# Performance work log

Hardware: AMD Instinct MI355X
Metric: run time of the kernel (lower is better)

Reference implementation:

```python
import jax, jax.numpy as jnp
import numpy as np
import math

B, L, S = 2, 2048, 2048
DIN, DK, DV, DOUT, H = 512, 512, 512, 512, 8
HEAD_SIZE = DK / H  # attention_head_size = dim_key_query_all / num_attention_heads


def setup_inputs() -> dict:
    key = jax.random.key(0)
    ks = jax.random.split(key, 12)
    inv = 1.0 / math.sqrt(DIN)
    return {
        "queries": jax.random.normal(ks[0], (B, L, DIN), jnp.float32),
        "keys": jax.random.normal(ks[1], (B, S, DIN), jnp.float32),
        "values": jax.random.normal(ks[2], (B, S, DIN), jnp.float32),
        "attn_mask": 0,
        "Wq": jax.random.uniform(ks[3], (DK, DIN), jnp.float32, -inv, inv),
        "Wk": jax.random.uniform(ks[4], (DK, DIN), jnp.float32, -inv, inv),
        "Wv": jax.random.uniform(ks[5], (DV, DIN), jnp.float32, -inv, inv),
        "bv": jax.random.uniform(ks[6], (DV,), jnp.float32, -inv, inv),
        "Wcb": jax.random.uniform(ks[7], (H, DIN), jnp.float32, -inv, inv),
        "mixing": 0.2 * jax.random.normal(ks[8], (H, DK), jnp.float32),
        "Wd": jax.random.uniform(ks[9], (DOUT, DV), jnp.float32, -1.0 / math.sqrt(DV), 1.0 / math.sqrt(DV)),
        "bd": jax.random.uniform(ks[10], (DOUT,), jnp.float32, -1.0 / math.sqrt(DV), 1.0 / math.sqrt(DV)),
    }


def reference(queries, keys, values, attn_mask, Wq, Wk, Wv, bv, Wcb, mixing, Wd, bd):
    # projections
    q = jnp.einsum('bld,ed->ble', queries, Wq)            # [B,L,DK]
    k = jnp.einsum('bsd,ed->bse', keys, Wk)               # [B,S,DK]
    v = jnp.einsum('bsd,ed->bse', values, Wv) + bv        # [B,S,DV]
    v = v.reshape(B, S, H, DV // H).transpose(0, 2, 1, 3)  # [B,H,S,dv]
    # collaborative scores: (q * mixing_h) @ k^T, per head
    mixed_q = q[:, None, :, :] * mixing[None, :, None, :]  # [B,H,L,DK]
    scores = jnp.einsum('bhle,bse->bhls', mixed_q, k)      # [B,H,L,S]
    # content bias: keys -> [B,S,H] -> broadcast over queries
    cb = jnp.einsum('bsd,hd->bhs', keys, Wcb)              # [B,H,S]
    scores = (scores + cb[:, :, None, :]) / math.sqrt(HEAD_SIZE)
    probs = jax.nn.softmax(scores, axis=-1)                # dropout p=0 (eval)
    ctx = jnp.einsum('bhls,bhsv->bhlv', probs, v)          # [B,H,L,dv]
    ctx = ctx.transpose(0, 2, 1, 3).reshape(B, L, DV)      # [B,L,DV]
    out = jnp.einsum('blv,ov->blo', ctx, Wd) + bd          # [B,L,DOUT]
    return out, probs
```

## Files before the change

kernel.cpp:

```cpp
#include <hip/hip_runtime.h>

typedef unsigned short u16;
typedef __bf16 bf16x8 __attribute__((ext_vector_type(8)));
typedef float floatx4 __attribute__((ext_vector_type(4)));

#define B_ 2
#define L_ 2048
#define S_ 2048
#define D_ 512
#define H_ 8

static __device__ __forceinline__ u16 f2bf(float f) {
  union { float f; unsigned u; } v; v.f = f;
  unsigned u = v.u;
  return (u16)((u + 0x7FFFu + ((u >> 16) & 1u)) >> 16);
}
static __device__ __forceinline__ float bf2f(u16 h) {
  union { unsigned u; float f; } v; v.u = ((unsigned)h) << 16;
  return v.f;
}

static __device__ __forceinline__ void gload16(const void* g, void* l) {
  __builtin_amdgcn_global_load_lds(
      (const __attribute__((address_space(1))) void*)g,
      (__attribute__((address_space(3))) void*)l, 16, 0, 0);
}

__global__ __launch_bounds__(256) void qkv_gemm(
    const float* __restrict__ Qin, const float* __restrict__ Kin, const float* __restrict__ Vin,
    const float* __restrict__ Wq, const float* __restrict__ Wk, const float* __restrict__ Wv,
    const float* __restrict__ bv,
    u16* __restrict__ qo, u16* __restrict__ ko, u16* __restrict__ vo)
{
  __shared__ u16 As[128][72];
  __shared__ u16 Bs[128][72];
  const int z = blockIdx.z;
  const float* A = (z == 0) ? Qin : (z == 1) ? Kin : Vin;
  const float* W = (z == 0) ? Wq : (z == 1) ? Wk : Wv;
  const int tid = threadIdx.x;
  const int m0 = blockIdx.y * 128;
  const int n0 = blockIdx.x * 128;
  const int lane = tid & 63, w = tid >> 6;
  const int ml = lane & 15, kl = lane >> 4;
  const int mqw = (w >> 1) * 64, nq = (w & 1) * 64;
  const int srow = tid >> 4, scg = tid & 15;

  floatx4 acc[4][4] = {};

  for (int k0 = 0; k0 < 512; k0 += 64) {
#pragma unroll
    for (int i = 0; i < 8; ++i) {
      const int r = srow + i * 16;
      float4 av = *(const float4*)&A[(size_t)(m0 + r) * 512 + k0 + scg * 4];
      ushort4 ua; ua.x = f2bf(av.x); ua.y = f2bf(av.y); ua.z = f2bf(av.z); ua.w = f2bf(av.w);
      *(ushort4*)&As[r][scg * 4] = ua;
      float4 wv = *(const float4*)&W[(size_t)(n0 + r) * 512 + k0 + scg * 4];
      ushort4 uw; uw.x = f2bf(wv.x); uw.y = f2bf(wv.y); uw.z = f2bf(wv.z); uw.w = f2bf(wv.w);
      *(ushort4*)&Bs[r][scg * 4] = uw;
    }
    __syncthreads();
#pragma unroll
    for (int kk = 0; kk < 64; kk += 32) {
      bf16x8 af[4], bfv[4];
#pragma unroll
      for (int i = 0; i < 4; ++i) af[i] = *(const bf16x8*)&As[mqw + i * 16 + ml][kk + kl * 8];
#pragma unroll
      for (int j = 0; j < 4; ++j) bfv[j] = *(const bf16x8*)&Bs[nq + j * 16 + ml][kk + kl * 8];
#pragma unroll
      for (int i = 0; i < 4; ++i)
#pragma unroll
        for (int j = 0; j < 4; ++j)
          acc[i][j] = __builtin_amdgcn_mfma_f32_16x16x32_bf16(af[i], bfv[j], acc[i][j], 0, 0, 0);
    }
    __syncthreads();
  }
#pragma unroll
  for (int i = 0; i < 4; ++i)
#pragma unroll
    for (int j = 0; j < 4; ++j) {
      const int gc = n0 + nq + j * 16 + ml;
#pragma unroll
      for (int r = 0; r < 4; ++r) {
        const int gr = m0 + mqw + i * 16 + kl * 4 + r;
        float v = acc[i][j][r];
        if (z == 0)      qo[(size_t)gr * 512 + gc] = f2bf(v);
        else if (z == 1) ko[(size_t)gr * 512 + gc] = f2bf(v);
        else             vo[(size_t)gr * 512 + gc] = f2bf(v + bv[gc]);
      }
    }
}

__global__ __launch_bounds__(256) void mixq_kernel(
    const u16* __restrict__ qb, const float* __restrict__ mixing, u16* __restrict__ mq)
{
  __shared__ float mixs[8 * 512];
  const int tid = threadIdx.x;
#pragma unroll
  for (int i = 0; i < 4; ++i)
    *(float4*)&mixs[(tid + i * 256) * 4] = *(const float4*)&mixing[(tid + i * 256) * 4];
  __syncthreads();
  const size_t unit = (size_t)blockIdx.x * 256 + tid;
  const size_t el = unit * 8;
  const int e = (int)(el & 511);
  const size_t bl = el >> 9;
  const int b = (int)(bl >> 11);
  const int l = (int)(bl & 2047);
  uint4 qv = *(const uint4*)&qb[el];
  const float q0 = bf2f((u16)(qv.x & 0xFFFFu)), q1 = bf2f((u16)(qv.x >> 16));
  const float q2 = bf2f((u16)(qv.y & 0xFFFFu)), q3 = bf2f((u16)(qv.y >> 16));
  const float q4 = bf2f((u16)(qv.z & 0xFFFFu)), q5 = bf2f((u16)(qv.z >> 16));
  const float q6 = bf2f((u16)(qv.w & 0xFFFFu)), q7 = bf2f((u16)(qv.w >> 16));
#pragma unroll
  for (int h = 0; h < 8; ++h) {
    const float* mp = &mixs[h * 512 + e];
    uint4 o;
    o.x = (unsigned)f2bf(q0 * mp[0]) | ((unsigned)f2bf(q1 * mp[1]) << 16);
    o.y = (unsigned)f2bf(q2 * mp[2]) | ((unsigned)f2bf(q3 * mp[3]) << 16);
    o.z = (unsigned)f2bf(q4 * mp[4]) | ((unsigned)f2bf(q5 * mp[5]) << 16);
    o.w = (unsigned)f2bf(q6 * mp[6]) | ((unsigned)f2bf(q7 * mp[7]) << 16);
    *(uint4*)&mq[(((size_t)b * 8 + h) * 2048 + l) * 512 + e] = o;
  }
}

__global__ __launch_bounds__(256) void out_gemm(
    const float* __restrict__ A0, const float* __restrict__ A1,
    const float* __restrict__ W,
    const float* __restrict__ bias, float* __restrict__ out)
{
  __shared__ u16 As[128][72];
  __shared__ u16 Bs[128][72];
  const int tid = threadIdx.x;
  const int m0 = blockIdx.y * 128;
  const int n0 = blockIdx.x * 128;
  const int lane = tid & 63, w = tid >> 6;
  const int ml = lane & 15, kl = lane >> 4;
  const int mqw = (w >> 1) * 64, nq = (w & 1) * 64;
  const int srow = tid >> 4, scg = tid & 15;

  floatx4 acc[4][4] = {};

  for (int k0 = 0; k0 < 512; k0 += 64) {
#pragma unroll
    for (int i = 0; i < 8; ++i) {
      const int r = srow + i * 16;
      const size_t aoff = (size_t)(m0 + r) * 512 + k0 + scg * 4;
      float4 a0 = *(const float4*)&A0[aoff];
      float4 a1 = *(const float4*)&A1[aoff];
      ushort4 ua;
      ua.x = f2bf(a0.x + a1.x); ua.y = f2bf(a0.y + a1.y);
      ua.z = f2bf(a0.z + a1.z); ua.w = f2bf(a0.w + a1.w);
      *(ushort4*)&As[r][scg * 4] = ua;
      float4 wv = *(const float4*)&W[(size_t)(n0 + r) * 512 + k0 + scg * 4];
      ushort4 uw; uw.x = f2bf(wv.x); uw.y = f2bf(wv.y); uw.z = f2bf(wv.z); uw.w = f2bf(wv.w);
      *(ushort4*)&Bs[r][scg * 4] = uw;
    }
    __syncthreads();
#pragma unroll
    for (int kk = 0; kk < 64; kk += 32) {
      bf16x8 af[4], bfv[4];
#pragma unroll
      for (int i = 0; i < 4; ++i) af[i] = *(const bf16x8*)&As[mqw + i * 16 + ml][kk + kl * 8];
#pragma unroll
      for (int j = 0; j < 4; ++j) bfv[j] = *(const bf16x8*)&Bs[nq + j * 16 + ml][kk + kl * 8];
#pragma unroll
      for (int i = 0; i < 4; ++i)
#pragma unroll
        for (int j = 0; j < 4; ++j)
          acc[i][j] = __builtin_amdgcn_mfma_f32_16x16x32_bf16(af[i], bfv[j], acc[i][j], 0, 0, 0);
    }
    __syncthreads();
  }
#pragma unroll
  for (int i = 0; i < 4; ++i)
#pragma unroll
    for (int j = 0; j < 4; ++j) {
      const int gc = n0 + nq + j * 16 + ml;
#pragma unroll
      for (int r = 0; r < 4; ++r) {
        const int gr = m0 + mqw + i * 16 + kl * 4 + r;
        out[(size_t)gr * 512 + gc] = acc[i][j][r] + bias[gc];
      }
    }
}

__global__ __launch_bounds__(256) void prep_kernel(
    const float* __restrict__ keys, const float* __restrict__ Wcb, float* __restrict__ cbuf,
    const u16* __restrict__ vb, u16* __restrict__ vT)
{
  __shared__ float Wl[8 * 512];
  __shared__ u16 t[64][72];
  const int tid = threadIdx.x;
  if (blockIdx.x < 1024) {
#pragma unroll
    for (int i = 0; i < 4; ++i) {
      const int idx = tid + i * 256;
      *(float4*)&Wl[idx * 4] = *(const float4*)&Wcb[idx * 4];
    }
    __syncthreads();
    const int w = tid >> 6, lane = tid & 63;
    const int rowid = blockIdx.x * 4 + w;
    const int b = rowid >> 11, s = rowid & 2047;
    const float* kr = keys + (size_t)rowid * 512;
    float acc[8] = {0.f, 0.f, 0.f, 0.f, 0.f, 0.f, 0.f, 0.f};
    for (int e = lane; e < 512; e += 64) {
      const float kv = kr[e];
#pragma unroll
      for (int hh = 0; hh < 8; ++hh) acc[hh] += kv * Wl[hh * 512 + e];
    }
#pragma unroll
    for (int hh = 0; hh < 8; ++hh) {
#pragma unroll
      for (int off = 32; off > 0; off >>= 1) acc[hh] += __shfl_xor(acc[hh], off, 64);
    }
    if (lane == 0) {
#pragma unroll
      for (int hh = 0; hh < 8; ++hh)
        cbuf[((size_t)b * 8 + hh) * 2048 + s] = acc[hh];
    }
  } else {
    const int id = blockIdx.x - 1024;
    const int b = id >> 8;
    const int rem = id & 255;
    const int s0 = (rem >> 3) * 64;
    const int e0 = (rem & 7) * 64;
    const int rr = tid >> 3, g = tid & 7;
#pragma unroll
    for (int i = 0; i < 2; ++i) {
      const int r = rr + i * 32;
      *(uint4*)&t[r][g * 8] = *(const uint4*)&vb[((size_t)b * S_ + s0 + r) * 512 + e0 + g * 8];
    }
    __syncthreads();
#pragma unroll
    for (int i = 0; i < 2; ++i) {
      const int er = rr + i * 32;
      uint4 o;
      o.x = (unsigned)t[g * 8 + 0][er] | ((unsigned)t[g * 8 + 1][er] << 16);
      o.y = (unsigned)t[g * 8 + 2][er] | ((unsigned)t[g * 8 + 3][er] << 16);
      o.z = (unsigned)t[g * 8 + 4][er] | ((unsigned)t[g * 8 + 5][er] << 16);
      o.w = (unsigned)t[g * 8 + 6][er] | ((unsigned)t[g * 8 + 7][er] << 16);
      *(uint4*)&vT[((size_t)b * 512 + e0 + er) * S_ + s0 + g * 8] = o;
    }
  }
}

template<int BF16OUT>
__global__ __launch_bounds__(256) void scores_gemm(
    const u16* __restrict__ mq, const u16* __restrict__ kb,
    const float* __restrict__ cbuf, float* __restrict__ sc, u16* __restrict__ sb)
{
  __shared__ u16 As[128][64];
  __shared__ u16 Bs[128][64];
  const int tid = threadIdx.x;
  const int bh = blockIdx.z, b = bh >> 3;
  const int m0 = blockIdx.y * 128;
  const int n0 = blockIdx.x * 128;
  const u16* mqb = mq + (size_t)bh * L_ * 512;
  const u16* kbb = kb + (size_t)b * S_ * 512;
  const int lane = tid & 63, w = tid >> 6;
  const int ml = lane & 15, kl = lane >> 4;
  const int mqw = (w >> 1) * 64, nq = (w & 1) * 64;
  const int lr = lane >> 3;
  const int lc = (lane & 7) * 8;

  floatx4 acc[4][4] = {};

  for (int k0 = 0; k0 < 512; k0 += 64) {
#pragma unroll
    for (int i = 0; i < 4; ++i) {
      const int c = w * 4 + i;
      const int r = c * 8 + lr;
      gload16(&mqb[(size_t)(m0 + r) * 512 + k0 + lc], &As[c * 8][0]);
      gload16(&kbb[(size_t)(n0 + r) * 512 + k0 + lc], &Bs[c * 8][0]);
    }
    __syncthreads();
#pragma unroll
    for (int kk = 0; kk < 64; kk += 32) {
      bf16x8 af[4], bfv[4];
#pragma unroll
      for (int i = 0; i < 4; ++i) af[i] = *(const bf16x8*)&As[mqw + i * 16 + ml][kk + kl * 8];
#pragma unroll
      for (int j = 0; j < 4; ++j) bfv[j] = *(const bf16x8*)&Bs[nq + j * 16 + ml][kk + kl * 8];
#pragma unroll
      for (int i = 0; i < 4; ++i)
#pragma unroll
        for (int j = 0; j < 4; ++j)
          acc[i][j] = __builtin_amdgcn_mfma_f32_16x16x32_bf16(af[i], bfv[j], acc[i][j], 0, 0, 0);
    }
    __syncthreads();
  }
  if constexpr (BF16OUT) {
    u16* outp = sb + ((size_t)bh * L_ + m0) * S_ + n0;
#pragma unroll
    for (int j = 0; j < 4; ++j) {
      const int gcl = nq + j * 16 + ml;
      const float cbv = cbuf[(size_t)bh * S_ + n0 + gcl];
#pragma unroll
      for (int i = 0; i < 4; ++i)
#pragma unroll
        for (int r = 0; r < 4; ++r) {
          const int grl = mqw + i * 16 + kl * 4 + r;
          outp[(size_t)grl * S_ + gcl] = f2bf((acc[i][j][r] + cbv) * 0.125f);
        }
    }
  } else {
    float* outp = sc + ((size_t)bh * L_ + m0) * S_ + n0;
#pragma unroll
    for (int j = 0; j < 4; ++j) {
      const int gcl = nq + j * 16 + ml;
      const float cbv = cbuf[(size_t)bh * S_ + n0 + gcl];
#pragma unroll
      for (int i = 0; i < 4; ++i)
#pragma unroll
        for (int r = 0; r < 4; ++r) {
          const int grl = mqw + i * 16 + kl * 4 + r;
          outp[(size_t)grl * S_ + gcl] = (acc[i][j][r] + cbv) * 0.125f;
        }
    }
  }
}

template<int BF16IN>
__global__ __launch_bounds__(256) void softmax_stream(
    u16* __restrict__ sb, float* probs)
{
  const int tid = threadIdx.x;
  const int row = blockIdx.x * 4 + (tid >> 6);
  const int lane = tid & 63;
  float s[32];
  if constexpr (BF16IN) {
    const u16* rp = sb + (size_t)row * 2048;
#pragma unroll
    for (int j = 0; j < 8; ++j) {
      uint2 v = *(const uint2*)&rp[lane * 4 + j * 256];
      s[4 * j + 0] = bf2f((u16)(v.x & 0xFFFFu));
      s[4 * j + 1] = bf2f((u16)(v.x >> 16));
      s[4 * j + 2] = bf2f((u16)(v.y & 0xFFFFu));
      s[4 * j + 3] = bf2f((u16)(v.y >> 16));
    }
  } else {
    const float* rp = probs + (size_t)row * 2048;
#pragma unroll
    for (int j = 0; j < 8; ++j) {
      float4 v = *(const float4*)&rp[lane * 4 + j * 256];
      s[4 * j + 0] = v.x; s[4 * j + 1] = v.y; s[4 * j + 2] = v.z; s[4 * j + 3] = v.w;
    }
  }
  float m = -3.0e38f;
#pragma unroll
  for (int i = 0; i < 32; ++i) m = fmaxf(m, s[i]);
#pragma unroll
  for (int off = 32; off > 0; off >>= 1) m = fmaxf(m, __shfl_xor(m, off, 64));
  float s0 = 0.f, s1 = 0.f, s2 = 0.f, s3 = 0.f;
#pragma unroll
  for (int i = 0; i < 32; i += 4) {
    s[i + 0] = __expf(s[i + 0] - m); s0 += s[i + 0];
    s[i + 1] = __expf(s[i + 1] - m); s1 += s[i + 1];
    s[i + 2] = __expf(s[i + 2] - m); s2 += s[i + 2];
    s[i + 3] = __expf(s[i + 3] - m); s3 += s[i + 3];
  }
  float sum = (s0 + s1) + (s2 + s3);
#pragma unroll
  for (int off = 32; off > 0; off >>= 1) sum += __shfl_xor(sum, off, 64);
  const float rl = 1.0f / sum;
  float* op = probs + (size_t)row * 2048;
  u16* bp = sb + (size_t)row * 2048;
#pragma unroll
  for (int j = 0; j < 8; ++j) {
    float4 o;
    o.x = s[4 * j + 0] * rl; o.y = s[4 * j + 1] * rl;
    o.z = s[4 * j + 2] * rl; o.w = s[4 * j + 3] * rl;
    *(float4*)&op[lane * 4 + j * 256] = o;
    if constexpr (BF16IN) {
      uint2 t;
      t.x = (unsigned)f2bf(o.x) | ((unsigned)f2bf(o.y) << 16);
      t.y = (unsigned)f2bf(o.z) | ((unsigned)f2bf(o.w) << 16);
      *(uint2*)&bp[lane * 4 + j * 256] = t;
    }
  }
}

template<int BF16IN>
__global__ __launch_bounds__(256) void ctx_gemm(
    const float* __restrict__ probsf, const u16* __restrict__ pb,
    const u16* __restrict__ vT, float* __restrict__ ctx0, float* __restrict__ ctx1)
{
  __shared__ u16 As[64][64];
  __shared__ u16 Bs[64][64];
  const int tid = threadIdx.x;
  const int kz = blockIdx.y;
  const int bh = blockIdx.z, b = bh >> 3, h = bh & 7;
  const int m0 = blockIdx.x * 64;
  const int lane = tid & 63, w = tid >> 6;
  const int ml = lane & 15, kl = lane >> 4;
  const int lr = lane >> 3;
  const int lc = (lane & 7) * 8;
  const u16* Ap = pb + ((size_t)bh * L_ + m0) * S_;
  const u16* Bp = vT + ((size_t)b * 512 + h * 64) * S_;

  floatx4 acc[4] = {};

  const int kend = kz * 1024 + 1024;
  for (int k0 = kz * 1024; k0 < kend; k0 += 64) {
    if constexpr (BF16IN) {
#pragma unroll
      for (int i = 0; i < 2; ++i) {
        const int c = w * 2 + i;
        const int r = c * 8 + lr;
        gload16(&Ap[(size_t)r * S_ + k0 + lc], &As[c * 8][0]);
        gload16(&Bp[(size_t)r * S_ + k0 + lc], &Bs[c * 8][0]);
      }
    } else {
      const int srow = tid >> 4, scg = tid & 15;
#pragma unroll
      for (int i = 0; i < 4; ++i) {
        const int r = srow + i * 16;
        float4 av = *(const float4*)&probsf[((size_t)bh * L_ + m0 + r) * S_ + k0 + scg * 4];
        ushort4 ua; ua.x = f2bf(av.x); ua.y = f2bf(av.y); ua.z = f2bf(av.z); ua.w = f2bf(av.w);
        *(ushort4*)&As[r][scg * 4] = ua;
      }
#pragma unroll
      for (int i = 0; i < 2; ++i) {
        const int c = w * 2 + i;
        const int r = c * 8 + lr;
        gload16(&Bp[(size_t)r * S_ + k0 + lc], &Bs[c * 8][0]);
      }
    }
    __syncthreads();
#pragma unroll
    for (int kk = 0; kk < 64; kk += 32) {
      bf16x8 af = *(const bf16x8*)&As[w * 16 + ml][kk + kl * 8];
#pragma unroll
      for (int j = 0; j < 4; ++j) {
        bf16x8 bfv = *(const bf16x8*)&Bs[j * 16 + ml][kk + kl * 8];
        acc[j] = __builtin_amdgcn_mfma_f32_16x16x32_bf16(af, bfv, acc[j], 0, 0, 0);
      }
    }
    __syncthreads();
  }
  float* cdst = kz ? ctx1 : ctx0;
#pragma unroll
  for (int j = 0; j < 4; ++j) {
    const int gc = h * 64 + j * 16 + ml;
#pragma unroll
    for (int r = 0; r < 4; ++r) {
      const int gl = m0 + w * 16 + kl * 4 + r;
      cdst[((size_t)b * L_ + gl) * 512 + gc] = acc[j][r];
    }
  }
}

extern "C" void kernel_launch(void* const* d_in, const int* in_sizes, int n_in,
                              void* d_out, int out_size, void* d_ws, size_t ws_size,
                              hipStream_t stream) {
  const float* queries = (const float*)d_in[0];
  const float* keys    = (const float*)d_in[1];
  const float* values  = (const float*)d_in[2];
  const float* Wq  = (const float*)d_in[4];
  const float* Wk  = (const float*)d_in[5];
  const float* Wv  = (const float*)d_in[6];
  const float* bv  = (const float*)d_in[7];
  const float* Wcb = (const float*)d_in[8];
  const float* mixing = (const float*)d_in[9];
  const float* Wd  = (const float*)d_in[10];
  const float* bd  = (const float*)d_in[11];

  float* out   = (float*)d_out;
  float* probs = out + (size_t)B_ * L_ * 512;

  char* ws = (char*)d_ws;
  u16*   qb  = (u16*)(ws);
  u16*   kb  = (u16*)(ws + (size_t)4  * 1024 * 1024);
  u16*   vb  = (u16*)(ws + (size_t)8  * 1024 * 1024);
  u16*   vT  = (u16*)(ws + (size_t)12 * 1024 * 1024);
  float* cbuf= (float*)(ws + (size_t)16 * 1024 * 1024);
  float* ctx0= (float*)(ws + (size_t)17 * 1024 * 1024);
  u16*   mq  = (u16*)(ws + (size_t)25 * 1024 * 1024);
  const size_t SB16_OFF = (size_t)57 * 1024 * 1024;
  const size_t SB16_SZ  = (size_t)B_ * H_ * L_ * S_ * 2;
  u16* sb16 = (u16*)(ws + SB16_OFF);
  const bool bigws = (ws_size >= SB16_OFF + SB16_SZ + (size_t)8 * 1024 * 1024);
  float* ctx1 = bigws ? (float*)(ws + SB16_OFF + SB16_SZ)
                      : (float*)(ws + SB16_OFF);

  hipLaunchKernelGGL(qkv_gemm, dim3(4, 32, 3), dim3(256), 0, stream,
                     queries, keys, values, Wq, Wk, Wv, bv, qb, kb, vb);
  hipLaunchKernelGGL(mixq_kernel, dim3(1024), dim3(256), 0, stream, qb, mixing, mq);
  hipLaunchKernelGGL(prep_kernel, dim3(1536), dim3(256), 0, stream,
                     keys, Wcb, cbuf, vb, vT);
  if (bigws) {
    hipLaunchKernelGGL(HIP_KERNEL_NAME(scores_gemm<1>), dim3(16, 16, 16), dim3(256), 0, stream,
                       mq, kb, cbuf, probs, sb16);
    hipLaunchKernelGGL(HIP_KERNEL_NAME(softmax_stream<1>), dim3(8192), dim3(256), 0, stream,
                       sb16, probs);
    hipLaunchKernelGGL(HIP_KERNEL_NAME(ctx_gemm<1>), dim3(32, 2, 16), dim3(256), 0, stream,
                       probs, sb16, vT, ctx0, ctx1);
  } else {
    hipLaunchKernelGGL(HIP_KERNEL_NAME(scores_gemm<0>), dim3(16, 16, 16), dim3(256), 0, stream,
                       mq, kb, cbuf, probs, sb16);
    hipLaunchKernelGGL(HIP_KERNEL_NAME(softmax_stream<0>), dim3(8192), dim3(256), 0, stream,
                       sb16, probs);
    hipLaunchKernelGGL(HIP_KERNEL_NAME(ctx_gemm<0>), dim3(32, 2, 16), dim3(256), 0, stream,
                       probs, sb16, vT, ctx0, ctx1);
  }
  hipLaunchKernelGGL(out_gemm, dim3(4, 32, 1), dim3(256), 0, stream,
                     ctx0, ctx1, Wd, bd, out);
}
```

Baseline: 563.5 us.

## Fuse softmax and context GEMM into one kernel with probs tile in LDS

Replaces the separate softmax and ctx GEMM kernels on the big-workspace path with one kernel. It loads 16 score rows into LDS, computes softmax, writes fp32 probs, keeps the bf16 probs in LDS and multiplies them by V directly. This removes the bf16 probs write-back and re-read and the split-K second ctx buffer, and lets out_gemm read a single ctx input. The cost is a 64KB+ LDS footprint per block, which limits occupancy, and each block re-streams V for only 16 rows with one MFMA chain per wave.

```diff
diff --git a/kernel.cpp b/kernel.cpp
--- a/kernel.cpp
+++ b/kernel.cpp
@@ -122,6 +122,7 @@
   }
 }
 
+template<int DUAL>
 __global__ __launch_bounds__(256) void out_gemm(
     const float* __restrict__ A0, const float* __restrict__ A1,
     const float* __restrict__ W,
@@ -145,10 +146,14 @@
       const int r = srow + i * 16;
       const size_t aoff = (size_t)(m0 + r) * 512 + k0 + scg * 4;
       float4 a0 = *(const float4*)&A0[aoff];
-      float4 a1 = *(const float4*)&A1[aoff];
       ushort4 ua;
-      ua.x = f2bf(a0.x + a1.x); ua.y = f2bf(a0.y + a1.y);
-      ua.z = f2bf(a0.z + a1.z); ua.w = f2bf(a0.w + a1.w);
+      if constexpr (DUAL) {
+        float4 a1 = *(const float4*)&A1[aoff];
+        ua.x = f2bf(a0.x + a1.x); ua.y = f2bf(a0.y + a1.y);
+        ua.z = f2bf(a0.z + a1.z); ua.w = f2bf(a0.w + a1.w);
+      } else {
+        ua.x = f2bf(a0.x); ua.y = f2bf(a0.y); ua.z = f2bf(a0.z); ua.w = f2bf(a0.w);
+      }
       *(ushort4*)&As[r][scg * 4] = ua;
       float4 wv = *(const float4*)&W[(size_t)(n0 + r) * 512 + k0 + scg * 4];
       ushort4 uw; uw.x = f2bf(wv.x); uw.y = f2bf(wv.y); uw.z = f2bf(wv.z); uw.w = f2bf(wv.w);
@@ -319,70 +324,144 @@
   }
 }
 
-template<int BF16IN>
-__global__ __launch_bounds__(256) void softmax_stream(
-    u16* __restrict__ sb, float* probs)
+__global__ __launch_bounds__(256) void smctx_fused(
+    const u16* __restrict__ sb, const u16* __restrict__ vT,
+    float* __restrict__ probs, float* __restrict__ ctx)
+{
+  __shared__ u16 P[16][2048];
+  __shared__ u16 Bs[64][64];
+  const int tid = threadIdx.x;
+  const int lane = tid & 63, w = tid >> 6;
+  const int bh = blockIdx.y, b = bh >> 3, h = bh & 7;
+  const int l0 = blockIdx.x * 16;
+
+  const u16* srow = sb + ((size_t)bh * L_ + l0) * S_;
+#pragma unroll
+  for (int i = 0; i < 16; ++i) {
+    const int ci = i * 4 + w;
+    const int r = ci >> 2;
+    const int cu = (ci & 3) * 512;
+    gload16(&srow[(size_t)r * S_ + cu + lane * 8], &P[r][cu]);
+  }
+  __syncthreads();
+
+  const int row = tid >> 4, seg = tid & 15;
+  const u16* prow_lds = &P[row][0];
+  float e[128];
+  float mx = -3.0e38f;
+#pragma unroll
+  for (int j = 0; j < 16; ++j) {
+    const int jc = (j + seg) & 15;
+    uint4 v = *(const uint4*)&prow_lds[seg * 128 + jc * 8];
+    const float f0 = bf2f((u16)(v.x & 0xFFFFu)), f1 = bf2f((u16)(v.x >> 16));
+    const float f2 = bf2f((u16)(v.y & 0xFFFFu)), f3 = bf2f((u16)(v.y >> 16));
+    const float f4 = bf2f((u16)(v.z & 0xFFFFu)), f5 = bf2f((u16)(v.z >> 16));
+    const float f6 = bf2f((u16)(v.w & 0xFFFFu)), f7 = bf2f((u16)(v.w >> 16));
+    e[j * 8 + 0] = f0; e[j * 8 + 1] = f1; e[j * 8 + 2] = f2; e[j * 8 + 3] = f3;
+    e[j * 8 + 4] = f4; e[j * 8 + 5] = f5; e[j * 8 + 6] = f6; e[j * 8 + 7] = f7;
+    mx = fmaxf(mx, fmaxf(fmaxf(f0, f1), fmaxf(f2, f3)));
+    mx = fmaxf(mx, fmaxf(fmaxf(f4, f5), fmaxf(f6, f7)));
+  }
+#pragma unroll
+  for (int off = 8; off > 0; off >>= 1) mx = fmaxf(mx, __shfl_xor(mx, off, 64));
+  float s0 = 0.f, s1 = 0.f, s2 = 0.f, s3 = 0.f;
+#pragma unroll
+  for (int i = 0; i < 128; i += 4) {
+    e[i + 0] = __expf(e[i + 0] - mx); s0 += e[i + 0];
+    e[i + 1] = __expf(e[i + 1] - mx); s1 += e[i + 1];
+    e[i + 2] = __expf(e[i + 2] - mx); s2 += e[i + 2];
+    e[i + 3] = __expf(e[i + 3] - mx); s3 += e[i + 3];
+  }
+  float sum = (s0 + s1) + (s2 + s3);
+#pragma unroll
+  for (int off = 8; off > 0; off >>= 1) sum += __shfl_xor(sum, off, 64);
+  const float rl = 1.0f / sum;
+
+  float* pout = probs + ((size_t)bh * L_ + l0 + row) * S_ + seg * 128;
+  u16* pl = &P[row][seg * 128];
+#pragma unroll
+  for (int j = 0; j < 16; ++j) {
+    const int jc = (j + seg) & 15;
+    float p0 = e[j * 8 + 0] * rl, p1 = e[j * 8 + 1] * rl;
+    float p2 = e[j * 8 + 2] * rl, p3 = e[j * 8 + 3] * rl;
+    float p4 = e[j * 8 + 4] * rl, p5 = e[j * 8 + 5] * rl;
+    float p6 = e[j * 8 + 6] * rl, p7 = e[j * 8 + 7] * rl;
+    float4 o0; o0.x = p0; o0.y = p1; o0.z = p2; o0.w = p3;
+    float4 o1; o1.x = p4; o1.y = p5; o1.z = p6; o1.w = p7;
+    *(float4*)&pout[jc * 8 + 0] = o0;
+    *(float4*)&pout[jc * 8 + 4] = o1;
+    uint4 t;
+    t.x = (unsigned)f2bf(p0) | ((unsigned)f2bf(p1) << 16);
+    t.y = (unsigned)f2bf(p2) | ((unsigned)f2bf(p3) << 16);
+    t.z = (unsigned)f2bf(p4) | ((unsigned)f2bf(p5) << 16);
+    t.w = (unsigned)f2bf(p6) | ((unsigned)f2bf(p7) << 16);
+    *(uint4*)&pl[jc * 8] = t;
+  }
+  __syncthreads();
+
+  const int ml = lane & 15, kl = lane >> 4;
+  const u16* vrow = vT + ((size_t)b * 512 + h * 64) * S_;
+  const int blr = lane >> 3;
+  const int blc = (lane & 7) * 8;
+  floatx4 acc = {};
+
+  for (int kc = 0; kc < 32; ++kc) {
+#pragma unroll
+    for (int i = 0; i < 2; ++i) {
+      const int c = w * 2 + i;
+      const int r = c * 8 + blr;
+      gload16(&vrow[(size_t)r * S_ + kc * 64 + blc], &Bs[c * 8][0]);
+    }
+    __syncthreads();
+#pragma unroll
+    for (int kk = 0; kk < 64; kk += 32) {
+      bf16x8 a  = *(const bf16x8*)&P[ml][kc * 64 + kk + kl * 8];
+      bf16x8 bb = *(const bf16x8*)&Bs[w * 16 + ml][kk + kl * 8];
+      acc = __builtin_amdgcn_mfma_f32_16x16x32_bf16(a, bb, acc, 0, 0, 0);
+    }
+    __syncthreads();
+  }
+#pragma unroll
+  for (int r = 0; r < 4; ++r)
+    ctx[((size_t)b * L_ + l0 + kl * 4 + r) * 512 + h * 64 + w * 16 + ml] = acc[r];
+}
+
+__global__ __launch_bounds__(256) void softmax_stream_f32(float* probs)
 {
   const int tid = threadIdx.x;
   const int row = blockIdx.x * 4 + (tid >> 6);
   const int lane = tid & 63;
   float s[32];
-  if constexpr (BF16IN) {
-    const u16* rp = sb + (size_t)row * 2048;
-#pragma unroll
-    for (int j = 0; j < 8; ++j) {
-      uint2 v = *(const uint2*)&rp[lane * 4 + j * 256];
-      s[4 * j + 0] = bf2f((u16)(v.x & 0xFFFFu));
-      s[4 * j + 1] = bf2f((u16)(v.x >> 16));
-      s[4 * j + 2] = bf2f((u16)(v.y & 0xFFFFu));
-      s[4 * j + 3] = bf2f((u16)(v.y >> 16));
-    }
-  } else {
-    const float* rp = probs + (size_t)row * 2048;
-#pragma unroll
-    for (int j = 0; j < 8; ++j) {
-      float4 v = *(const float4*)&rp[lane * 4 + j * 256];
-      s[4 * j + 0] = v.x; s[4 * j + 1] = v.y; s[4 * j + 2] = v.z; s[4 * j + 3] = v.w;
-    }
+  const float* rp = probs + (size_t)row * 2048;
+#pragma unroll
+  for (int j = 0; j < 8; ++j) {
+    float4 v = *(const float4*)&rp[lane * 4 + j * 256];
+    s[4 * j + 0] = v.x; s[4 * j + 1] = v.y; s[4 * j + 2] = v.z; s[4 * j + 3] = v.w;
   }
   float m = -3.0e38f;
 #pragma unroll
   for (int i = 0; i < 32; ++i) m = fmaxf(m, s[i]);
 #pragma unroll
   for (int off = 32; off > 0; off >>= 1) m = fmaxf(m, __shfl_xor(m, off, 64));
-  float s0 = 0.f, s1 = 0.f, s2 = 0.f, s3 = 0.f;
-#pragma unroll
-  for (int i = 0; i < 32; i += 4) {
-    s[i + 0] = __expf(s[i + 0] - m); s0 += s[i + 0];
-    s[i + 1] = __expf(s[i + 1] - m); s1 += s[i + 1];
-    s[i + 2] = __expf(s[i + 2] - m); s2 += s[i + 2];
-    s[i + 3] = __expf(s[i + 3] - m); s3 += s[i + 3];
-  }
-  float sum = (s0 + s1) + (s2 + s3);
-#pragma unroll
-  for (int off = 32; off > 0; off >>= 1) sum += __shfl_xor(sum, off, 64);
-  const float rl = 1.0f / sum;
+  float s0 = 0.f;
+#pragma unroll
+  for (int i = 0; i < 32; ++i) { s[i] = __expf(s[i] - m); s0 += s[i]; }
+#pragma unroll
+  for (int off = 32; off > 0; off >>= 1) s0 += __shfl_xor(s0, off, 64);
+  const float rl = 1.0f / s0;
   float* op = probs + (size_t)row * 2048;
-  u16* bp = sb + (size_t)row * 2048;
 #pragma unroll
   for (int j = 0; j < 8; ++j) {
     float4 o;
     o.x = s[4 * j + 0] * rl; o.y = s[4 * j + 1] * rl;
     o.z = s[4 * j + 2] * rl; o.w = s[4 * j + 3] * rl;
     *(float4*)&op[lane * 4 + j * 256] = o;
-    if constexpr (BF16IN) {
-      uint2 t;
-      t.x = (unsigned)f2bf(o.x) | ((unsigned)f2bf(o.y) << 16);
-      t.y = (unsigned)f2bf(o.z) | ((unsigned)f2bf(o.w) << 16);
-      *(uint2*)&bp[lane * 4 + j * 256] = t;
-    }
-  }
-}
-
-template<int BF16IN>
-__global__ __launch_bounds__(256) void ctx_gemm(
-    const float* __restrict__ probsf, const u16* __restrict__ pb,
-    const u16* __restrict__ vT, float* __restrict__ ctx0, float* __restrict__ ctx1)
+  }
+}
+
+__global__ __launch_bounds__(256) void ctx_gemm_f32(
+    const float* __restrict__ probsf, const u16* __restrict__ vT,
+    float* __restrict__ ctx0, float* __restrict__ ctx1)
 {
   __shared__ u16 As[64][64];
   __shared__ u16 Bs[64][64];
@@ -394,36 +473,25 @@
   const int ml = lane & 15, kl = lane >> 4;
   const int lr = lane >> 3;
   const int lc = (lane & 7) * 8;
-  const u16* Ap = pb + ((size_t)bh * L_ + m0) * S_;
   const u16* Bp = vT + ((size_t)b * 512 + h * 64) * S_;
 
   floatx4 acc[4] = {};
 
   const int kend = kz * 1024 + 1024;
   for (int k0 = kz * 1024; k0 < kend; k0 += 64) {
-    if constexpr (BF16IN) {
-#pragma unroll
-      for (int i = 0; i < 2; ++i) {
-        const int c = w * 2 + i;
-        const int r = c * 8 + lr;
-        gload16(&Ap[(size_t)r * S_ + k0 + lc], &As[c * 8][0]);
-        gload16(&Bp[(size_t)r * S_ + k0 + lc], &Bs[c * 8][0]);
-      }
-    } else {
-      const int srow = tid >> 4, scg = tid & 15;
-#pragma unroll
-      for (int i = 0; i < 4; ++i) {
-        const int r = srow + i * 16;
-        float4 av = *(const float4*)&probsf[((size_t)bh * L_ + m0 + r) * S_ + k0 + scg * 4];
-        ushort4 ua; ua.x = f2bf(av.x); ua.y = f2bf(av.y); ua.z = f2bf(av.z); ua.w = f2bf(av.w);
-        *(ushort4*)&As[r][scg * 4] = ua;
-      }
-#pragma unroll
-      for (int i = 0; i < 2; ++i) {
-        const int c = w * 2 + i;
-        const int r = c * 8 + lr;
-        gload16(&Bp[(size_t)r * S_ + k0 + lc], &Bs[c * 8][0]);
-      }
+    const int srow = tid >> 4, scg = tid & 15;
+#pragma unroll
+    for (int i = 0; i < 4; ++i) {
+      const int r = srow + i * 16;
+      float4 av = *(const float4*)&probsf[((size_t)bh * L_ + m0 + r) * S_ + k0 + scg * 4];
+      ushort4 ua; ua.x = f2bf(av.x); ua.y = f2bf(av.y); ua.z = f2bf(av.z); ua.w = f2bf(av.w);
+      *(ushort4*)&As[r][scg * 4] = ua;
+    }
+#pragma unroll
+    for (int i = 0; i < 2; ++i) {
+      const int c = w * 2 + i;
+      const int r = c * 8 + lr;
+      gload16(&Bp[(size_t)r * S_ + k0 + lc], &Bs[c * 8][0]);
     }
     __syncthreads();
 #pragma unroll
@@ -490,18 +558,17 @@
   if (bigws) {
     hipLaunchKernelGGL(HIP_KERNEL_NAME(scores_gemm<1>), dim3(16, 16, 16), dim3(256), 0, stream,
                        mq, kb, cbuf, probs, sb16);
-    hipLaunchKernelGGL(HIP_KERNEL_NAME(softmax_stream<1>), dim3(8192), dim3(256), 0, stream,
-                       sb16, probs);
-    hipLaunchKernelGGL(HIP_KERNEL_NAME(ctx_gemm<1>), dim3(32, 2, 16), dim3(256), 0, stream,
-                       probs, sb16, vT, ctx0, ctx1);
+    hipLaunchKernelGGL(smctx_fused, dim3(128, 16), dim3(256), 0, stream,
+                       sb16, vT, probs, ctx0);
+    hipLaunchKernelGGL(HIP_KERNEL_NAME(out_gemm<0>), dim3(4, 32, 1), dim3(256), 0, stream,
+                       ctx0, ctx1, Wd, bd, out);
   } else {
     hipLaunchKernelGGL(HIP_KERNEL_NAME(scores_gemm<0>), dim3(16, 16, 16), dim3(256), 0, stream,
                        mq, kb, cbuf, probs, sb16);
-    hipLaunchKernelGGL(HIP_KERNEL_NAME(softmax_stream<0>), dim3(8192), dim3(256), 0, stream,
-                       sb16, probs);
-    hipLaunchKernelGGL(HIP_KERNEL_NAME(ctx_gemm<0>), dim3(32, 2, 16), dim3(256), 0, stream,
-                       probs, sb16, vT, ctx0, ctx1);
-  }
-  hipLaunchKernelGGL(out_gemm, dim3(4, 32, 1), dim3(256), 0, stream,
-                     ctx0, ctx1, Wd, bd, out);
-}
+    hipLaunchKernelGGL(softmax_stream_f32, dim3(8192), dim3(256), 0, stream, probs);
+    hipLaunchKernelGGL(ctx_gemm_f32, dim3(32, 2, 16), dim3(256), 0, stream,
+                       probs, vT, ctx0, ctx1);
+    hipLaunchKernelGGL(HIP_KERNEL_NAME(out_gemm<1>), dim3(4, 32, 1), dim3(256), 0, stream,
+                       ctx0, ctx1, Wd, bd, out);
+  }
+}
```

Measured after the change: 690.1 us. +22.5%, slower.
